# Performance work log

Measured on AMD Instinct MI355X. Metric: run time of the kernel, lower is better.

Reference implementation:

```python
import jax, jax.numpy as jnp
import numpy as np

WINDOW = 1024


def _dft_weights(window):
    # w[k, n] = exp(-2*pi*i*k*n/window); torch module stores real/imag parts as conv weights
    n = np.arange(window)
    ang = -2.0 * np.pi * (n[:, None] * n[None, :]) / window  # [K, N] in float64 like numpy
    return np.cos(ang).astype(np.float32), np.sin(ang).astype(np.float32)


def setup_inputs() -> dict:
    key = jax.random.key(0)
    k1, k2, k3, k4 = jax.random.split(key, 4)
    w_real, w_imag = _dft_weights(WINDOW)
    bound = 1.0 / np.sqrt(WINDOW)  # torch Conv1d default bias init: U(-1/sqrt(fan_in), 1/sqrt(fan_in))
    return {
        "x_r": jax.random.normal(k1, (8, 4096, WINDOW), dtype=jnp.float32),
        "x_i": jax.random.normal(k2, (8, 4096, WINDOW), dtype=jnp.float32),
        "w_real": jnp.asarray(w_real),
        "w_imag": jnp.asarray(w_imag),
        "b_real": jax.random.uniform(k3, (WINDOW,), minval=-bound, maxval=bound, dtype=jnp.float32),
        "b_imag": jax.random.uniform(k4, (WINDOW,), minval=-bound, maxval=bound, dtype=jnp.float32),
    }


def reference(x_r, x_i, w_real, w_imag, b_real, b_imag):
    # Conv1d with full-window kernel == matmul over the last axis.
    # conv_real(x) = x @ w_real.T + b_real ; conv_imag(x) = x @ w_imag.T + b_imag
    xr_wr = jnp.einsum('bfn,kn->bfk', x_r, w_real)
    xr_wi = jnp.einsum('bfn,kn->bfk', x_r, w_imag)
    xi_wr = jnp.einsum('bfn,kn->bfk', x_i, w_real)
    xi_wi = jnp.einsum('bfn,kn->bfk', x_i, w_imag)
    real = (xr_wr + b_real) - (xi_wi + b_imag)
    imag = (xr_wi + b_imag) + (xi_wr + b_real)
    return (real, imag)
```

## Files before the change

### kernel.cpp

```cpp
#include <hip/hip_runtime.h>
#include <stdint.h>

#define NFFT  1024
#define MROWS 32768
#define RPB   8
#define PADN  1088

__device__ __forceinline__ int P(int a) { return a + (a >> 4); }

__device__ __forceinline__ void dft4(float (&vr)[4], float (&vi)[4]) {
  const float t0r = vr[0] + vr[2], t0i = vi[0] + vi[2];
  const float t1r = vr[0] - vr[2], t1i = vi[0] - vi[2];
  const float t2r = vr[1] + vr[3], t2i = vi[1] + vi[3];
  const float t3r = vi[1] - vi[3], t3i = vr[3] - vr[1];
  vr[0] = t0r + t2r; vi[0] = t0i + t2i;
  vr[1] = t1r + t3r; vi[1] = t1i + t3i;
  vr[2] = t0r - t2r; vi[2] = t0i - t2i;
  vr[3] = t1r - t3r; vi[3] = t1i - t3i;
}

template<int NS, int STEP>
__device__ __forceinline__ void lds_stage(int j,
    const float* __restrict__ sr, const float* __restrict__ si,
    float* __restrict__ dr, float* __restrict__ di,
    const float* __restrict__ twr, const float* __restrict__ twi) {
  float vr[4], vi[4];
#pragma unroll
  for (int r = 0; r < 4; ++r) {
    vr[r] = sr[P(j + 256 * r)];
    vi[r] = si[P(j + 256 * r)];
  }
  const int m = j & (NS - 1);
#pragma unroll
  for (int r = 1; r < 4; ++r) {
    const int idx = P(r * m * STEP);
    const float c = twr[idx], d = twi[idx];
    const float nr = vr[r] * c - vi[r] * d;
    const float ni = vr[r] * d + vi[r] * c;
    vr[r] = nr; vi[r] = ni;
  }
  dft4(vr, vi);
  const int base = ((j & ~(NS - 1)) << 2) + m;
#pragma unroll
  for (int r = 0; r < 4; ++r) {
    dr[P(base + r * NS)] = vr[r];
    di[P(base + r * NS)] = vi[r];
  }
  __syncthreads();
}

__global__ void __launch_bounds__(256)
fft1024(const float* __restrict__ xr, const float* __restrict__ xi,
        const float* __restrict__ wr, const float* __restrict__ wi,
        const float* __restrict__ br, const float* __restrict__ bi,
        float* __restrict__ out) {
  __shared__ float twr[PADN], twi[PADN];
  __shared__ float d0r[PADN], d0i[PADN], d1r[PADN], d1i[PADN];

  const int j = threadIdx.x;

  {
    const float4 cr = *(const float4*)(wr + NFFT + 4 * j);
    const float4 ci = *(const float4*)(wi + NFFT + 4 * j);
    twr[P(4 * j + 0)] = cr.x; twr[P(4 * j + 1)] = cr.y;
    twr[P(4 * j + 2)] = cr.z; twr[P(4 * j + 3)] = cr.w;
    twi[P(4 * j + 0)] = ci.x; twi[P(4 * j + 1)] = ci.y;
    twi[P(4 * j + 2)] = ci.z; twi[P(4 * j + 3)] = ci.w;
  }

  float badd_r[4], badd_i[4];
#pragma unroll
  for (int r = 0; r < 4; ++r) {
    const int c = j + 256 * r;
    const float a = br[c], b = bi[c];
    badd_r[r] = a - b;
    badd_i[r] = a + b;
  }

  const int row0 = blockIdx.x * RPB;
  for (int rr = 0; rr < RPB; ++rr) {
    const size_t row = (size_t)(row0 + rr);
    const float* pr = xr + row * NFFT;
    const float* pi = xi + row * NFFT;

    float vr[4], vi[4];
#pragma unroll
    for (int r = 0; r < 4; ++r) {
      vr[r] = pr[j + 256 * r];
      vi[r] = pi[j + 256 * r];
    }
    dft4(vr, vi);
#pragma unroll
    for (int r = 0; r < 4; ++r) {
      d1r[P(4 * j + r)] = vr[r];
      d1i[P(4 * j + r)] = vi[r];
    }
    __syncthreads();

    lds_stage<4, 64>(j, d1r, d1i, d0r, d0i, twr, twi);
    lds_stage<16, 16>(j, d0r, d0i, d1r, d1i, twr, twi);
    lds_stage<64, 4>(j, d1r, d1i, d0r, d0i, twr, twi);

#pragma unroll
    for (int r = 0; r < 4; ++r) {
      vr[r] = d0r[P(j + 256 * r)];
      vi[r] = d0i[P(j + 256 * r)];
    }
#pragma unroll
    for (int r = 1; r < 4; ++r) {
      const int idx = P(r * j);
      const float c = twr[idx], d = twi[idx];
      const float nr = vr[r] * c - vi[r] * d;
      const float ni = vr[r] * d + vi[r] * c;
      vr[r] = nr; vi[r] = ni;
    }
    dft4(vr, vi);
    float* o_r = out + row * NFFT;
    float* o_i = out + (size_t)MROWS * NFFT + row * NFFT;
#pragma unroll
    for (int r = 0; r < 4; ++r) {
      const int c = j + 256 * r;
      o_r[c] = vr[r] + badd_r[r];
      o_i[c] = vi[r] + badd_i[r];
    }
  }
}

extern "C" void kernel_launch(void* const* d_in, const int* in_sizes, int n_in,
                              void* d_out, int out_size, void* d_ws, size_t ws_size,
                              hipStream_t stream) {
  const float* xr = (const float*)d_in[0];
  const float* xi = (const float*)d_in[1];
  const float* wr = (const float*)d_in[2];
  const float* wi = (const float*)d_in[3];
  const float* br = (const float*)d_in[4];
  const float* bi = (const float*)d_in[5];
  float* out = (float*)d_out;
  (void)in_sizes; (void)n_in; (void)out_size; (void)d_ws; (void)ws_size;

  fft1024<<<MROWS / RPB, 256, 0, stream>>>(xr, xi, wr, wi, br, bi, out);
}
```

Measured before the change: 452.9 us.

## Compute one FFT row per wavefront with register radix-16 passes

Restructures the 1024-point FFT so each 64-lane wavefront owns a whole row. Each lane holds 16 complex values in registers and runs two radix-4 stages per LDS exchange, with twiddles preloaded into registers. This replaces the block-wide __syncthreads and five LDS round trips with two wave-local interleaved float2 exchanges. It also uses a persistent grid-stride loop and float4 output stores. The cost is heavy register pressure (launch bounds 256,3), and correctness relies on wavefront lockstep instead of explicit barriers.

Result: slower. 602.4 us (+33.0%).

```diff
diff --git a/kernel.cpp b/kernel.cpp
--- a/kernel.cpp
+++ b/kernel.cpp
@@ -3,125 +3,175 @@
 
 #define NFFT  1024
 #define MROWS 32768
-#define RPB   8
-#define PADN  1088
+#define GRID  2048
 
-__device__ __forceinline__ int P(int a) { return a + (a >> 4); }
+__device__ __forceinline__ int Pc(int i) { return i + (i >> 4); }
 
-__device__ __forceinline__ void dft4(float (&vr)[4], float (&vi)[4]) {
-  const float t0r = vr[0] + vr[2], t0i = vi[0] + vi[2];
-  const float t1r = vr[0] - vr[2], t1i = vi[0] - vi[2];
-  const float t2r = vr[1] + vr[3], t2i = vi[1] + vi[3];
-  const float t3r = vi[1] - vi[3], t3i = vr[3] - vr[1];
-  vr[0] = t0r + t2r; vi[0] = t0i + t2i;
-  vr[1] = t1r + t3r; vi[1] = t1i + t3i;
-  vr[2] = t0r - t2r; vi[2] = t0i - t2i;
-  vr[3] = t1r - t3r; vi[3] = t1i - t3i;
+__device__ __forceinline__ void dft4(float& ar, float& ai, float& br_, float& bi_,
+                                     float& cr, float& ci, float& dr, float& di) {
+  const float t0r = ar + cr,  t0i = ai + ci;
+  const float t1r = ar - cr,  t1i = ai - ci;
+  const float t2r = br_ + dr, t2i = bi_ + di;
+  const float t3r = bi_ - di, t3i = dr - br_;
+  ar  = t0r + t2r; ai  = t0i + t2i;
+  br_ = t1r + t3r; bi_ = t1i + t3i;
+  cr  = t0r - t2r; ci  = t0i - t2i;
+  dr  = t1r - t3r; di  = t1i - t3i;
 }
 
-template<int NS, int STEP>
-__device__ __forceinline__ void lds_stage(int j,
-    const float* __restrict__ sr, const float* __restrict__ si,
-    float* __restrict__ dr, float* __restrict__ di,
-    const float* __restrict__ twr, const float* __restrict__ twi) {
-  float vr[4], vi[4];
-#pragma unroll
-  for (int r = 0; r < 4; ++r) {
-    vr[r] = sr[P(j + 256 * r)];
-    vi[r] = si[P(j + 256 * r)];
-  }
-  const int m = j & (NS - 1);
-#pragma unroll
-  for (int r = 1; r < 4; ++r) {
-    const int idx = P(r * m * STEP);
-    const float c = twr[idx], d = twi[idx];
-    const float nr = vr[r] * c - vi[r] * d;
-    const float ni = vr[r] * d + vi[r] * c;
-    vr[r] = nr; vi[r] = ni;
-  }
-  dft4(vr, vi);
-  const int base = ((j & ~(NS - 1)) << 2) + m;
-#pragma unroll
-  for (int r = 0; r < 4; ++r) {
-    dr[P(base + r * NS)] = vr[r];
-    di[P(base + r * NS)] = vi[r];
-  }
-  __syncthreads();
+__device__ __forceinline__ void cmul(float& xr, float& xi, float c, float s) {
+  const float r = xr * c - xi * s;
+  xi = xr * s + xi * c;
+  xr = r;
 }
 
-__global__ void __launch_bounds__(256)
+__global__ void __launch_bounds__(256, 3)
 fft1024(const float* __restrict__ xr, const float* __restrict__ xi,
         const float* __restrict__ wr, const float* __restrict__ wi,
         const float* __restrict__ br, const float* __restrict__ bi,
         float* __restrict__ out) {
-  __shared__ float twr[PADN], twi[PADN];
-  __shared__ float d0r[PADN], d0i[PADN], d1r[PADN], d1i[PADN];
+  __shared__ float lds[4 * 2176];
+  const int tid = threadIdx.x;
+  const int w   = tid >> 6;
+  const int t   = tid & 63;
+  float* buf = lds + w * 2176;
+  const int b = t & 15;
+  const int a = t >> 4;
 
-  const int j = threadIdx.x;
+  const float* tgr = wr + NFFT;
+  const float* tgi = wi + NFFT;
 
+  float T1r[10], T1i[10];
+#pragma unroll
+  for (int z = 0; z < 10; ++z) { T1r[z] = 1.f; T1i[z] = 0.f; }
   {
-    const float4 cr = *(const float4*)(wr + NFFT + 4 * j);
-    const float4 ci = *(const float4*)(wi + NFFT + 4 * j);
-    twr[P(4 * j + 0)] = cr.x; twr[P(4 * j + 1)] = cr.y;
-    twr[P(4 * j + 2)] = cr.z; twr[P(4 * j + 3)] = cr.w;
-    twi[P(4 * j + 0)] = ci.x; twi[P(4 * j + 1)] = ci.y;
-    twi[P(4 * j + 2)] = ci.z; twi[P(4 * j + 3)] = ci.w;
+    const int zs[6] = {1, 2, 3, 4, 6, 9};
+#pragma unroll
+    for (int u = 0; u < 6; ++u) {
+      T1r[zs[u]] = tgr[64 * zs[u]];
+      T1i[zs[u]] = tgi[64 * zs[u]];
+    }
+  }
+  float T2r[4], T2i[4];
+#pragma unroll
+  for (int r = 1; r < 4; ++r) { T2r[r] = tgr[16 * r * b]; T2i[r] = tgi[16 * r * b]; }
+  float T3r[4][4], T3i[4][4];
+#pragma unroll
+  for (int q = 1; q < 4; ++q)
+#pragma unroll
+    for (int k = 0; k < 4; ++k) {
+      const int e = 4 * q * (b + 16 * k);
+      T3r[q][k] = tgr[e]; T3i[q][k] = tgi[e];
+    }
+  float T4r[4][4], T4i[4][4];
+#pragma unroll
+  for (int m = 0; m < 4; ++m)
+#pragma unroll
+    for (int r = 1; r < 4; ++r) {
+      const int e = r * (4 * t + m);
+      T4r[m][r] = tgr[e]; T4i[m][r] = tgi[e];
+    }
+
+  float badd_r[4][4], badd_i[4][4];
+#pragma unroll
+  for (int k = 0; k < 4; ++k) {
+    const float4 fb = *(const float4*)(br + 4 * t + 256 * k);
+    const float4 gb = *(const float4*)(bi + 4 * t + 256 * k);
+    badd_r[k][0] = fb.x - gb.x; badd_i[k][0] = fb.x + gb.x;
+    badd_r[k][1] = fb.y - gb.y; badd_i[k][1] = fb.y + gb.y;
+    badd_r[k][2] = fb.z - gb.z; badd_i[k][2] = fb.z + gb.z;
+    badd_r[k][3] = fb.w - gb.w; badd_i[k][3] = fb.w + gb.w;
   }
 
-  float badd_r[4], badd_i[4];
+  for (int row = blockIdx.x * 4 + w; row < MROWS; row += GRID * 4) {
+    const float* pr = xr + (size_t)row * NFFT;
+    const float* px = xi + (size_t)row * NFFT;
+
+    float vr[16], vi[16];
 #pragma unroll
-  for (int r = 0; r < 4; ++r) {
-    const int c = j + 256 * r;
-    const float a = br[c], b = bi[c];
-    badd_r[r] = a - b;
-    badd_i[r] = a + b;
-  }
-
-  const int row0 = blockIdx.x * RPB;
-  for (int rr = 0; rr < RPB; ++rr) {
-    const size_t row = (size_t)(row0 + rr);
-    const float* pr = xr + row * NFFT;
-    const float* pi = xi + row * NFFT;
-
-    float vr[4], vi[4];
-#pragma unroll
-    for (int r = 0; r < 4; ++r) {
-      vr[r] = pr[j + 256 * r];
-      vi[r] = pi[j + 256 * r];
-    }
-    dft4(vr, vi);
-#pragma unroll
-    for (int r = 0; r < 4; ++r) {
-      d1r[P(4 * j + r)] = vr[r];
-      d1i[P(4 * j + r)] = vi[r];
-    }
-    __syncthreads();
-
-    lds_stage<4, 64>(j, d1r, d1i, d0r, d0i, twr, twi);
-    lds_stage<16, 16>(j, d0r, d0i, d1r, d1i, twr, twi);
-    lds_stage<64, 4>(j, d1r, d1i, d0r, d0i, twr, twi);
+    for (int e = 0; e < 16; ++e) { vr[e] = pr[t + 64 * e]; vi[e] = px[t + 64 * e]; }
 
 #pragma unroll
-    for (int r = 0; r < 4; ++r) {
-      vr[r] = d0r[P(j + 256 * r)];
-      vi[r] = d0i[P(j + 256 * r)];
+    for (int q = 0; q < 4; ++q)
+      dft4(vr[q], vi[q], vr[q + 4], vi[q + 4], vr[q + 8], vi[q + 8], vr[q + 12], vi[q + 12]);
+
+#pragma unroll
+    for (int m = 0; m < 4; ++m) {
+      if (m > 0) {
+#pragma unroll
+        for (int q = 1; q < 4; ++q)
+          cmul(vr[q + 4 * m], vi[q + 4 * m], T1r[q * m], T1i[q * m]);
+      }
+      dft4(vr[4 * m], vi[4 * m], vr[1 + 4 * m], vi[1 + 4 * m],
+           vr[2 + 4 * m], vi[2 + 4 * m], vr[3 + 4 * m], vi[3 + 4 * m]);
     }
+
 #pragma unroll
-    for (int r = 1; r < 4; ++r) {
-      const int idx = P(r * j);
-      const float c = twr[idx], d = twi[idx];
-      const float nr = vr[r] * c - vi[r] * d;
-      const float ni = vr[r] * d + vi[r] * c;
-      vr[r] = nr; vi[r] = ni;
+    for (int u = 0; u < 16; ++u) {
+      const int m = u & 3, k1 = u >> 2;
+      *(float2*)&buf[2 * Pc(16 * t + u)] = make_float2(vr[k1 + 4 * m], vi[k1 + 4 * m]);
     }
-    dft4(vr, vi);
-    float* o_r = out + row * NFFT;
-    float* o_i = out + (size_t)MROWS * NFFT + row * NFFT;
+    asm volatile("" ::: "memory");
+
 #pragma unroll
-    for (int r = 0; r < 4; ++r) {
-      const int c = j + 256 * r;
-      o_r[c] = vr[r] + badd_r[r];
-      o_i[c] = vi[r] + badd_i[r];
+    for (int q = 0; q < 4; ++q)
+#pragma unroll
+      for (int r = 0; r < 4; ++r) {
+        const float2 f = *(const float2*)&buf[2 * Pc(t + 64 * q + 256 * r)];
+        vr[q + 4 * r] = f.x; vi[q + 4 * r] = f.y;
+      }
+#pragma unroll
+    for (int q = 0; q < 4; ++q) {
+#pragma unroll
+      for (int r = 1; r < 4; ++r)
+        cmul(vr[q + 4 * r], vi[q + 4 * r], T2r[r], T2i[r]);
+      dft4(vr[q], vi[q], vr[q + 4], vi[q + 4], vr[q + 8], vi[q + 8], vr[q + 12], vi[q + 12]);
+    }
+
+#pragma unroll
+    for (int k2 = 0; k2 < 4; ++k2) {
+#pragma unroll
+      for (int q = 1; q < 4; ++q)
+        cmul(vr[q + 4 * k2], vi[q + 4 * k2], T3r[q][k2], T3i[q][k2]);
+      dft4(vr[4 * k2], vi[4 * k2], vr[1 + 4 * k2], vi[1 + 4 * k2],
+           vr[2 + 4 * k2], vi[2 + 4 * k2], vr[3 + 4 * k2], vi[3 + 4 * k2]);
+    }
+
+#pragma unroll
+    for (int k2 = 0; k2 < 4; ++k2)
+#pragma unroll
+      for (int k3 = 0; k3 < 4; ++k3)
+        *(float2*)&buf[2 * Pc(256 * a + b + 16 * k2 + 64 * k3)] =
+            make_float2(vr[k3 + 4 * k2], vi[k3 + 4 * k2]);
+    asm volatile("" ::: "memory");
+
+#pragma unroll
+    for (int m = 0; m < 4; ++m)
+#pragma unroll
+      for (int r = 0; r < 4; ++r) {
+        const float2 f = *(const float2*)&buf[2 * Pc(4 * t + m + 256 * r)];
+        vr[m + 4 * r] = f.x; vi[m + 4 * r] = f.y;
+      }
+    asm volatile("" ::: "memory");
+#pragma unroll
+    for (int m = 0; m < 4; ++m) {
+#pragma unroll
+      for (int r = 1; r < 4; ++r)
+        cmul(vr[m + 4 * r], vi[m + 4 * r], T4r[m][r], T4i[m][r]);
+      dft4(vr[m], vi[m], vr[m + 4], vi[m + 4], vr[m + 8], vi[m + 8], vr[m + 12], vi[m + 12]);
+    }
+
+    float* o_r = out + (size_t)row * NFFT;
+    float* o_i = out + (size_t)MROWS * NFFT + (size_t)row * NFFT;
+#pragma unroll
+    for (int k = 0; k < 4; ++k) {
+      float4 R, I;
+      R.x = vr[0 + 4 * k] + badd_r[k][0]; I.x = vi[0 + 4 * k] + badd_i[k][0];
+      R.y = vr[1 + 4 * k] + badd_r[k][1]; I.y = vi[1 + 4 * k] + badd_i[k][1];
+      R.z = vr[2 + 4 * k] + badd_r[k][2]; I.z = vi[2 + 4 * k] + badd_i[k][2];
+      R.w = vr[3 + 4 * k] + badd_r[k][3]; I.w = vi[3 + 4 * k] + badd_i[k][3];
+      *(float4*)(o_r + 4 * t + 256 * k) = R;
+      *(float4*)(o_i + 4 * t + 256 * k) = I;
     }
   }
 }
@@ -138,5 +188,5 @@
   float* out = (float*)d_out;
   (void)in_sizes; (void)n_in; (void)out_size; (void)d_ws; (void)ws_size;
 
-  fft1024<<<MROWS / RPB, 256, 0, stream>>>(xr, xi, wr, wi, br, bi, out);
+  fft1024<<<GRID, 256, 0, stream>>>(xr, xi, wr, wi, br, bi, out);
 }
```
